# Kernel optimization log

Measured on AMD Instinct MI355X. Metric: run time of the kernel, lower is better.

## Reference

```python
import jax, jax.numpy as jnp
import numpy as np

N = 100000      # nodes
E = 640000      # edges
VOCAB = 100     # Embedding(num_embeddings=100)
EMB = 10        # embed_dim
H = 128         # GCN hidden width


def gcn_conv(x, W, b, src, dst, n):
    """PyG GCNConv: linear (no bias) -> add self loops -> sym-normalized scatter-add -> +bias."""
    x = x @ W                                  # [n, out]
    loop = jnp.arange(n, dtype=src.dtype)
    src2 = jnp.concatenate([src, loop])        # [E+n]
    dst2 = jnp.concatenate([dst, loop])
    deg = jax.ops.segment_sum(jnp.ones_like(dst2, dtype=x.dtype), dst2, num_segments=n)
    dinv = jnp.where(deg > 0, jax.lax.rsqrt(deg), 0.0)
    norm = dinv[src2] * dinv[dst2]             # [E+n]
    out = jax.ops.segment_sum(x[src2] * norm[:, None], dst2, num_segments=n)
    return out + b


def setup_inputs() -> dict:
    key = jax.random.key(0)
    ks = jax.random.split(key, 9)
    x = jax.random.randint(ks[0], (N, 1), 0, VOCAB, dtype=jnp.int32)
    edge_index = jax.random.randint(ks[1], (2, E), 0, N, dtype=jnp.int32)
    batch = jnp.zeros((N,), dtype=jnp.int32)
    emb = jax.random.normal(ks[2], (VOCAB, EMB), dtype=jnp.float32)
    W1 = jax.random.normal(ks[3], (EMB, H), dtype=jnp.float32) * 0.1
    b1 = jnp.zeros((H,), dtype=jnp.float32)
    W2 = jax.random.normal(ks[4], (H, H), dtype=jnp.float32) * 0.1
    b2 = jnp.zeros((H,), dtype=jnp.float32)
    W3 = jax.random.normal(ks[5], (H, 1), dtype=jnp.float32) * 0.1
    b3 = jnp.zeros((1,), dtype=jnp.float32)
    return {"x": x, "edge_index": edge_index, "batch": batch,
            "emb": emb, "W1": W1, "b1": b1, "W2": W2, "b2": b2, "W3": W3, "b3": b3}


def reference(x, edge_index, batch, emb, W1, b1, W2, b2, W3, b3):
    # eval mode: dropout(p=0.5) is identity
    h = emb[x[:, 0]]                           # [N, EMB] embedding lookup + squeeze
    src, dst = edge_index[0], edge_index[1]
    n = h.shape[0]
    h = jax.nn.relu(gcn_conv(h, W1, b1, src, dst, n))   # [N, 128]
    h = jax.nn.relu(gcn_conv(h, W2, b2, src, dst, n))   # [N, 128]
    out = jax.nn.sigmoid((h @ W3 + b3).reshape(-1))      # [N]
    return out
```

## Files before the change

kernel.cpp:

```cpp
#include <hip/hip_runtime.h>
#include <math.h>

#define HDIM 128
#define EMBD 10
#define CAP  64
#define ZSTRIDE 136

typedef __attribute__((ext_vector_type(8))) short short8;
typedef __attribute__((ext_vector_type(8))) unsigned short ushort8;
typedef __attribute__((ext_vector_type(4))) float float4a;
typedef __attribute__((ext_vector_type(4))) unsigned uint4a;

__device__ inline ushort bf16_rne(float f) {
    unsigned u = __float_as_uint(f);
    unsigned r = (u + 0x7fffu + ((u >> 16) & 1u)) >> 16;
    return (ushort)r;
}
__device__ inline float bf16_to_f(ushort u) {
    return __uint_as_float(((unsigned)u) << 16);
}
__device__ inline void acc_row(float* acc, uint4a y, float wt) {
#pragma unroll
    for (int i = 0; i < 4; ++i) {
        unsigned u = y[i];
        acc[2 * i]     += wt * __uint_as_float(u << 16);
        acc[2 * i + 1] += wt * __uint_as_float(u & 0xffff0000u);
    }
}

__global__ void k_prep(const float* __restrict__ emb, const float* __restrict__ W1,
                       const float* __restrict__ W2, ushort* __restrict__ Tb,
                       ushort* __restrict__ W2t, int* __restrict__ cnt,
                       int N, int vocab) {
    int t = blockIdx.x * 256 + threadIdx.x;
    if (t < N) cnt[t] = 0;
    if (t < vocab * HDIM) {
        int c = t >> 7, f = t & 127;
        float s = 0.f;
#pragma unroll
        for (int k = 0; k < EMBD; ++k) s += emb[c * EMBD + k] * W1[k * HDIM + f];
        Tb[t] = bf16_rne(s);
    }
    if (t < HDIM * HDIM) {
        int n = t >> 7, k = t & 127;
        W2t[t] = bf16_rne(W2[k * HDIM + n]);
    }
}

__global__ void k_fill(const int* __restrict__ src, const int* __restrict__ dst,
                       int* __restrict__ cnt, int* __restrict__ slot, int E) {
    int e = blockIdx.x * blockDim.x + threadIdx.x;
    if (e >= E) return;
    int d = dst[e];
    int p = atomicAdd(&cnt[d], 1);
    if (p < CAP) slot[(size_t)d * CAP + p] = src[e];
}

__global__ void k_meta(const int* __restrict__ x, const int* __restrict__ cnt,
                       unsigned* __restrict__ meta, int N) {
    int v = blockIdx.x * 256 + threadIdx.x;
    if (v >= N) return;
    meta[v] = ((unsigned)x[v] << 16) | (unsigned)bf16_rne(rsqrtf((float)cnt[v] + 1.0f));
}

__global__ __launch_bounds__(512) void k_gather1(const int* __restrict__ slot,
                                                 const int* __restrict__ cnt,
                                                 const unsigned* __restrict__ meta,
                                                 const ushort* __restrict__ Tb,
                                                 const float* __restrict__ b1,
                                                 ushort* __restrict__ Ap,
                                                 int N, int vocab) {
    __shared__ ushort TbL[100 * HDIM];
    int n8 = (vocab * HDIM) >> 3;
    for (int i = threadIdx.x; i < n8; i += 512)
        ((ushort8*)TbL)[i] = ((const ushort8*)Tb)[i];
    __syncthreads();

    int tid = blockIdx.x * 512 + threadIdx.x;
    int v = tid >> 4, q = tid & 15;
    if (v >= N) return;
    int deg = cnt[v];
    int m = min(deg, CAP);
    float dv = rsqrtf((float)deg + 1.0f);
    int total = m + 1;
    const int* slotv = slot + (size_t)v * CAP;

    float acc[8] = {0.f, 0.f, 0.f, 0.f, 0.f, 0.f, 0.f, 0.f};
    for (int base = 0; base < total; base += 8) {
        int4 sa = *(const int4*)(slotv + base);
        int4 sb = *(const int4*)(slotv + base + 4);
        int sv[8] = {sa.x, sa.y, sa.z, sa.w, sb.x, sb.y, sb.z, sb.w};
        const unsigned* mp[8];
#pragma unroll
        for (int t = 0; t < 8; ++t) {
            int idx = base + t;
            mp[t] = meta + ((idx < m) ? sv[t] : v);
        }
        unsigned m0, m1, m2, m3, m4, m5, m6, m7;
        asm volatile(
            "global_load_dword %0, %8, off\n\t"
            "global_load_dword %1, %9, off\n\t"
            "global_load_dword %2, %10, off\n\t"
            "global_load_dword %3, %11, off\n\t"
            "global_load_dword %4, %12, off\n\t"
            "global_load_dword %5, %13, off\n\t"
            "global_load_dword %6, %14, off\n\t"
            "global_load_dword %7, %15, off\n\t"
            "s_waitcnt vmcnt(0)"
            : "=&v"(m0), "=&v"(m1), "=&v"(m2), "=&v"(m3),
              "=&v"(m4), "=&v"(m5), "=&v"(m6), "=&v"(m7)
            : "v"(mp[0]), "v"(mp[1]), "v"(mp[2]), "v"(mp[3]),
              "v"(mp[4]), "v"(mp[5]), "v"(mp[6]), "v"(mp[7]));
        unsigned mm[8] = {m0, m1, m2, m3, m4, m5, m6, m7};
#pragma unroll
        for (int t = 0; t < 8; ++t) {
            float wt = (base + t <= m) ? bf16_to_f((ushort)(mm[t] & 0xffffu)) : 0.f;
            ushort8 y = *(const ushort8*)&TbL[(mm[t] >> 16) * HDIM + q * 8];
#pragma unroll
            for (int k = 0; k < 8; ++k) acc[k] += wt * bf16_to_f(y[k]);
        }
    }
    float4 bb0 = *(const float4*)(b1 + q * 8);
    float4 bb1 = *(const float4*)(b1 + q * 8 + 4);
    float bb[8] = {bb0.x, bb0.y, bb0.z, bb0.w, bb1.x, bb1.y, bb1.z, bb1.w};
    ushort8 o;
#pragma unroll
    for (int k = 0; k < 8; ++k)
        o[k] = bf16_rne(dv * fmaxf(dv * acc[k] + bb[k], 0.f));
    *(ushort8*)(Ap + (size_t)v * HDIM + q * 8) = o;
}

__global__ __launch_bounds__(256, 4) void k_conv2(const int* __restrict__ slot,
                                                  const int* __restrict__ cnt,
                                                  const ushort* __restrict__ Ap,
                                                  const ushort* __restrict__ W2t,
                                                  const float* __restrict__ b2,
                                                  const float* __restrict__ W3,
                                                  const float* __restrict__ b3,
                                                  float* __restrict__ out, int N) {
    __shared__ ushort Z[16 * ZSTRIDE];
    __shared__ float pbuf[4][16];
    int tid = threadIdx.x;
    int g = tid >> 4, q = tid & 15;
    int v0 = blockIdx.x * 16;
    int v = min(v0 + g, N - 1);

    int deg = cnt[v];
    int m = min(deg, CAP);
    float dv = rsqrtf((float)deg + 1.0f);
    int total = m + 1;
    const int* slotv = slot + (size_t)v * CAP;
    const ushort* aq = Ap + q * 8;

    float acc[8] = {0.f, 0.f, 0.f, 0.f, 0.f, 0.f, 0.f, 0.f};
    for (int base = 0; base < total; base += 8) {
        int4 sa = *(const int4*)(slotv + base);
        int4 sb = *(const int4*)(slotv + base + 4);
        int sv[8] = {sa.x, sa.y, sa.z, sa.w, sb.x, sb.y, sb.z, sb.w};
        const ushort* pp[8];
#pragma unroll
        for (int t = 0; t < 8; ++t) {
            int idx = base + t;
            int s = (idx < m) ? sv[t] : v;
            pp[t] = aq + (size_t)s * HDIM;
        }
        uint4a r0, r1, r2, r3, r4, r5, r6, r7;
        asm volatile(
            "global_load_dwordx4 %0, %8, off\n\t"
            "global_load_dwordx4 %1, %9, off\n\t"
            "global_load_dwordx4 %2, %10, off\n\t"
            "global_load_dwordx4 %3, %11, off\n\t"
            "global_load_dwordx4 %4, %12, off\n\t"
            "global_load_dwordx4 %5, %13, off\n\t"
            "global_load_dwordx4 %6, %14, off\n\t"
            "global_load_dwordx4 %7, %15, off\n\t"
            "s_waitcnt vmcnt(0)"
            : "=&v"(r0), "=&v"(r1), "=&v"(r2), "=&v"(r3),
              "=&v"(r4), "=&v"(r5), "=&v"(r6), "=&v"(r7)
            : "v"(pp[0]), "v"(pp[1]), "v"(pp[2]), "v"(pp[3]),
              "v"(pp[4]), "v"(pp[5]), "v"(pp[6]), "v"(pp[7]));
        acc_row(acc, r0, (base + 0 <= m) ? 1.f : 0.f);
        acc_row(acc, r1, (base + 1 <= m) ? 1.f : 0.f);
        acc_row(acc, r2, (base + 2 <= m) ? 1.f : 0.f);
        acc_row(acc, r3, (base + 3 <= m) ? 1.f : 0.f);
        acc_row(acc, r4, (base + 4 <= m) ? 1.f : 0.f);
        acc_row(acc, r5, (base + 5 <= m) ? 1.f : 0.f);
        acc_row(acc, r6, (base + 6 <= m) ? 1.f : 0.f);
        acc_row(acc, r7, (base + 7 <= m) ? 1.f : 0.f);
    }
    ushort8 z;
#pragma unroll
    for (int k = 0; k < 8; ++k) z[k] = bf16_rne(dv * acc[k]);
    *(ushort8*)&Z[g * ZSTRIDE + q * 8] = z;
    __syncthreads();

    int lane = tid & 63, w = tid >> 6;
    int l15 = lane & 15, g4 = lane >> 4;
    short8 af[4];
#pragma unroll
    for (int kt = 0; kt < 4; ++kt)
        af[kt] = *(const short8*)&Z[l15 * ZSTRIDE + kt * 32 + g4 * 8];

    float pr[4] = {0.f, 0.f, 0.f, 0.f};
#pragma unroll
    for (int i = 0; i < 2; ++i) {
        int nt = w * 2 + i;
        int col = nt * 16 + l15;
        const ushort* bp = W2t + (size_t)col * HDIM + g4 * 8;
        float4a accD = {0.f, 0.f, 0.f, 0.f};
#pragma unroll
        for (int kt = 0; kt < 4; ++kt) {
            short8 bf = *(const short8*)(bp + kt * 32);
            accD = __builtin_amdgcn_mfma_f32_16x16x32_bf16(af[kt], bf, accD, 0, 0, 0);
        }
        float bc = b2[col], wc = W3[col];
#pragma unroll
        for (int r = 0; r < 4; ++r)
            pr[r] += fmaxf(accD[r] + bc, 0.f) * wc;
    }
#pragma unroll
    for (int off = 1; off < 16; off <<= 1) {
#pragma unroll
        for (int r = 0; r < 4; ++r) pr[r] += __shfl_xor(pr[r], off, 16);
    }
    if (l15 == 0) {
#pragma unroll
        for (int r = 0; r < 4; ++r) pbuf[w][g4 * 4 + r] = pr[r];
    }
    __syncthreads();
    if (tid < 16) {
        int row = tid;
        float s = pbuf[0][row] + pbuf[1][row] + pbuf[2][row] + pbuf[3][row];
        int vr = v0 + row;
        if (vr < N) out[vr] = 1.f / (1.f + expf(-(s + b3[0])));
    }
}

extern "C" void kernel_launch(void* const* d_in, const int* in_sizes, int n_in,
                              void* d_out, int out_size, void* d_ws, size_t ws_size,
                              hipStream_t stream) {
    const int*   x    = (const int*)d_in[0];
    const int*   ei   = (const int*)d_in[1];
    const float* emb  = (const float*)d_in[3];
    const float* W1   = (const float*)d_in[4];
    const float* b1   = (const float*)d_in[5];
    const float* W2   = (const float*)d_in[6];
    const float* b2   = (const float*)d_in[7];
    const float* W3   = (const float*)d_in[8];
    const float* b3   = (const float*)d_in[9];
    float*       out  = (float*)d_out;

    int N = in_sizes[0];
    int E = in_sizes[1] / 2;
    int vocab = in_sizes[3] / EMBD;
    const int* src = ei;
    const int* dst = ei + E;

    char* w = (char*)d_ws;
    ushort*   Tb   = (ushort*)w;    w += (size_t)vocab * HDIM * 2;
    ushort*   Ap   = (ushort*)w;    w += (size_t)N * HDIM * 2;
    ushort*   W2t  = (ushort*)w;    w += (size_t)HDIM * HDIM * 2;
    int*      cnt  = (int*)w;       w += (size_t)N * 4;
    unsigned* meta = (unsigned*)w;  w += (size_t)N * 4;
    int*      slot = (int*)w;       w += (size_t)N * CAP * 4 + 64;

    int prep_elems = N;
    if (vocab * HDIM > prep_elems) prep_elems = vocab * HDIM;
    if (HDIM * HDIM > prep_elems) prep_elems = HDIM * HDIM;
    k_prep<<<(prep_elems + 255) / 256, 256, 0, stream>>>(emb, W1, W2, Tb, W2t, cnt, N, vocab);
    k_fill<<<(E + 255) / 256, 256, 0, stream>>>(src, dst, cnt, slot, E);
    k_meta<<<(N + 255) / 256, 256, 0, stream>>>(x, cnt, meta, N);

    int g1blocks = (int)(((long long)N * 16 + 511) / 512);
    k_gather1<<<g1blocks, 512, 0, stream>>>(slot, cnt, meta, Tb, b1, Ap, N, vocab);

    int cblocks = (N + 15) / 16;
    k_conv2<<<cblocks, 256, 0, stream>>>(slot, cnt, Ap, W2t, b2, W3, b3, out, N);
}
```

Before: 182.0 us.

## Replace fixed-capacity neighbor slots with compact CSR built by prefix scan

Replaces the per-node 64-entry slot buckets with an exact CSR adjacency. It is built by an atomic degree count, a three-kernel prefix scan (which also writes the per-node meta word) and an atomic fill pass that yields per-node end offsets. The gather kernels read neighbor indices from the compact CSR array instead of the sparse padded slot table. This shrinks the adjacency footprint and removes the degree cap, but adds an extra pass over edges and several small launches.

```diff
diff --git a/kernel.cpp b/kernel.cpp
--- a/kernel.cpp
+++ b/kernel.cpp
@@ -3,7 +3,6 @@
 
 #define HDIM 128
 #define EMBD 10
-#define CAP  64
 #define ZSTRIDE 136
 
 typedef __attribute__((ext_vector_type(8))) short short8;
@@ -30,10 +29,10 @@
 
 __global__ void k_prep(const float* __restrict__ emb, const float* __restrict__ W1,
                        const float* __restrict__ W2, ushort* __restrict__ Tb,
-                       ushort* __restrict__ W2t, int* __restrict__ cnt,
+                       ushort* __restrict__ W2t, int* __restrict__ deg,
                        int N, int vocab) {
     int t = blockIdx.x * 256 + threadIdx.x;
-    if (t < N) cnt[t] = 0;
+    if (t < N) deg[t] = 0;
     if (t < vocab * HDIM) {
         int c = t >> 7, f = t & 127;
         float s = 0.f;
@@ -47,24 +46,63 @@
     }
 }
 
+__global__ void k_degcount(const int* __restrict__ dst, int* __restrict__ deg, int E) {
+    int i = blockIdx.x * blockDim.x + threadIdx.x;
+    if (i < E) atomicAdd(&deg[dst[i]], 1);
+}
+
+__global__ void k_psum1(int* __restrict__ a, int* __restrict__ partial,
+                        const int* __restrict__ x, unsigned* __restrict__ meta, int N) {
+    __shared__ int sh[256];
+    int t = threadIdx.x;
+    int i = blockIdx.x * 256 + t;
+    int v = (i < N) ? a[i] : 0;
+    if (i < N)
+        meta[i] = ((unsigned)x[i] << 16) | (unsigned)bf16_rne(rsqrtf((float)v + 1.0f));
+    sh[t] = v;
+    __syncthreads();
+#pragma unroll
+    for (int off = 1; off < 256; off <<= 1) {
+        int add = (t >= off) ? sh[t - off] : 0;
+        __syncthreads();
+        sh[t] += add;
+        __syncthreads();
+    }
+    if (i < N) a[i] = sh[t] - v;
+    if (t == 255) partial[blockIdx.x] = sh[255];
+}
+
+__global__ void k_psum2(int* __restrict__ partial, int nb) {
+    __shared__ int sh[512];
+    int t = threadIdx.x;
+    int v = (t < nb) ? partial[t] : 0;
+    sh[t] = v;
+    __syncthreads();
+#pragma unroll
+    for (int off = 1; off < 512; off <<= 1) {
+        int add = (t >= off) ? sh[t - off] : 0;
+        __syncthreads();
+        sh[t] += add;
+        __syncthreads();
+    }
+    if (t < nb) partial[t] = sh[t] - v;
+}
+
+__global__ void k_psum3(int* __restrict__ a, const int* __restrict__ partial, int N) {
+    int i = blockIdx.x * 256 + threadIdx.x;
+    if (i < N) a[i] += partial[blockIdx.x];
+}
+
 __global__ void k_fill(const int* __restrict__ src, const int* __restrict__ dst,
-                       int* __restrict__ cnt, int* __restrict__ slot, int E) {
+                       int* __restrict__ ends, int* __restrict__ csr, int E) {
     int e = blockIdx.x * blockDim.x + threadIdx.x;
     if (e >= E) return;
-    int d = dst[e];
-    int p = atomicAdd(&cnt[d], 1);
-    if (p < CAP) slot[(size_t)d * CAP + p] = src[e];
-}
-
-__global__ void k_meta(const int* __restrict__ x, const int* __restrict__ cnt,
-                       unsigned* __restrict__ meta, int N) {
-    int v = blockIdx.x * 256 + threadIdx.x;
-    if (v >= N) return;
-    meta[v] = ((unsigned)x[v] << 16) | (unsigned)bf16_rne(rsqrtf((float)cnt[v] + 1.0f));
-}
-
-__global__ __launch_bounds__(512) void k_gather1(const int* __restrict__ slot,
-                                                 const int* __restrict__ cnt,
+    int p = atomicAdd(&ends[dst[e]], 1);
+    csr[p] = src[e];
+}
+
+__global__ __launch_bounds__(512) void k_gather1(const int* __restrict__ csr,
+                                                 const int* __restrict__ ends,
                                                  const unsigned* __restrict__ meta,
                                                  const ushort* __restrict__ Tb,
                                                  const float* __restrict__ b1,
@@ -79,22 +117,20 @@
     int tid = blockIdx.x * 512 + threadIdx.x;
     int v = tid >> 4, q = tid & 15;
     if (v >= N) return;
-    int deg = cnt[v];
-    int m = min(deg, CAP);
+    int e1 = ends[v];
+    int e0 = (v == 0) ? 0 : ends[v - 1];
+    int deg = e1 - e0;
     float dv = rsqrtf((float)deg + 1.0f);
-    int total = m + 1;
-    const int* slotv = slot + (size_t)v * CAP;
+    int total = deg + 1;
 
     float acc[8] = {0.f, 0.f, 0.f, 0.f, 0.f, 0.f, 0.f, 0.f};
     for (int base = 0; base < total; base += 8) {
-        int4 sa = *(const int4*)(slotv + base);
-        int4 sb = *(const int4*)(slotv + base + 4);
-        int sv[8] = {sa.x, sa.y, sa.z, sa.w, sb.x, sb.y, sb.z, sb.w};
         const unsigned* mp[8];
 #pragma unroll
         for (int t = 0; t < 8; ++t) {
             int idx = base + t;
-            mp[t] = meta + ((idx < m) ? sv[t] : v);
+            int s = csr[e0 + idx];
+            mp[t] = meta + ((idx < deg) ? s : v);
         }
         unsigned m0, m1, m2, m3, m4, m5, m6, m7;
         asm volatile(
@@ -114,7 +150,7 @@
         unsigned mm[8] = {m0, m1, m2, m3, m4, m5, m6, m7};
 #pragma unroll
         for (int t = 0; t < 8; ++t) {
-            float wt = (base + t <= m) ? bf16_to_f((ushort)(mm[t] & 0xffffu)) : 0.f;
+            float wt = (base + t <= deg) ? bf16_to_f((ushort)(mm[t] & 0xffffu)) : 0.f;
             ushort8 y = *(const ushort8*)&TbL[(mm[t] >> 16) * HDIM + q * 8];
 #pragma unroll
             for (int k = 0; k < 8; ++k) acc[k] += wt * bf16_to_f(y[k]);
@@ -130,8 +166,8 @@
     *(ushort8*)(Ap + (size_t)v * HDIM + q * 8) = o;
 }
 
-__global__ __launch_bounds__(256, 4) void k_conv2(const int* __restrict__ slot,
-                                                  const int* __restrict__ cnt,
+__global__ __launch_bounds__(256, 4) void k_conv2(const int* __restrict__ csr,
+                                                  const int* __restrict__ ends,
                                                   const ushort* __restrict__ Ap,
                                                   const ushort* __restrict__ W2t,
                                                   const float* __restrict__ b2,
@@ -145,23 +181,21 @@
     int v0 = blockIdx.x * 16;
     int v = min(v0 + g, N - 1);
 
-    int deg = cnt[v];
-    int m = min(deg, CAP);
+    int e1 = ends[v];
+    int e0 = (v == 0) ? 0 : ends[v - 1];
+    int deg = e1 - e0;
     float dv = rsqrtf((float)deg + 1.0f);
-    int total = m + 1;
-    const int* slotv = slot + (size_t)v * CAP;
+    int total = deg + 1;
     const ushort* aq = Ap + q * 8;
 
     float acc[8] = {0.f, 0.f, 0.f, 0.f, 0.f, 0.f, 0.f, 0.f};
     for (int base = 0; base < total; base += 8) {
-        int4 sa = *(const int4*)(slotv + base);
-        int4 sb = *(const int4*)(slotv + base + 4);
-        int sv[8] = {sa.x, sa.y, sa.z, sa.w, sb.x, sb.y, sb.z, sb.w};
         const ushort* pp[8];
 #pragma unroll
         for (int t = 0; t < 8; ++t) {
             int idx = base + t;
-            int s = (idx < m) ? sv[t] : v;
+            int s = csr[e0 + idx];
+            s = (idx < deg) ? s : v;
             pp[t] = aq + (size_t)s * HDIM;
         }
         uint4a r0, r1, r2, r3, r4, r5, r6, r7;
@@ -179,14 +213,14 @@
               "=&v"(r4), "=&v"(r5), "=&v"(r6), "=&v"(r7)
             : "v"(pp[0]), "v"(pp[1]), "v"(pp[2]), "v"(pp[3]),
               "v"(pp[4]), "v"(pp[5]), "v"(pp[6]), "v"(pp[7]));
-        acc_row(acc, r0, (base + 0 <= m) ? 1.f : 0.f);
-        acc_row(acc, r1, (base + 1 <= m) ? 1.f : 0.f);
-        acc_row(acc, r2, (base + 2 <= m) ? 1.f : 0.f);
-        acc_row(acc, r3, (base + 3 <= m) ? 1.f : 0.f);
-        acc_row(acc, r4, (base + 4 <= m) ? 1.f : 0.f);
-        acc_row(acc, r5, (base + 5 <= m) ? 1.f : 0.f);
-        acc_row(acc, r6, (base + 6 <= m) ? 1.f : 0.f);
-        acc_row(acc, r7, (base + 7 <= m) ? 1.f : 0.f);
+        acc_row(acc, r0, (base + 0 <= deg) ? 1.f : 0.f);
+        acc_row(acc, r1, (base + 1 <= deg) ? 1.f : 0.f);
+        acc_row(acc, r2, (base + 2 <= deg) ? 1.f : 0.f);
+        acc_row(acc, r3, (base + 3 <= deg) ? 1.f : 0.f);
+        acc_row(acc, r4, (base + 4 <= deg) ? 1.f : 0.f);
+        acc_row(acc, r5, (base + 5 <= deg) ? 1.f : 0.f);
+        acc_row(acc, r6, (base + 6 <= deg) ? 1.f : 0.f);
+        acc_row(acc, r7, (base + 7 <= deg) ? 1.f : 0.f);
     }
     ushort8 z;
 #pragma unroll
@@ -257,23 +291,29 @@
     const int* dst = ei + E;
 
     char* w = (char*)d_ws;
-    ushort*   Tb   = (ushort*)w;    w += (size_t)vocab * HDIM * 2;
-    ushort*   Ap   = (ushort*)w;    w += (size_t)N * HDIM * 2;
-    ushort*   W2t  = (ushort*)w;    w += (size_t)HDIM * HDIM * 2;
-    int*      cnt  = (int*)w;       w += (size_t)N * 4;
-    unsigned* meta = (unsigned*)w;  w += (size_t)N * 4;
-    int*      slot = (int*)w;       w += (size_t)N * CAP * 4 + 64;
-
+    ushort*   Tb      = (ushort*)w;    w += (size_t)vocab * HDIM * 2;
+    ushort*   Ap      = (ushort*)w;    w += (size_t)N * HDIM * 2;
+    ushort*   W2t     = (ushort*)w;    w += (size_t)HDIM * HDIM * 2;
+    int*      ends    = (int*)w;       w += (size_t)N * 4;
+    unsigned* meta    = (unsigned*)w;  w += (size_t)N * 4;
+    int*      partial = (int*)w;       w += 512 * 4;
+    int*      csr     = (int*)w;       w += ((size_t)E + 16) * 4;
+
+    int nb = (N + 255) / 256;
     int prep_elems = N;
     if (vocab * HDIM > prep_elems) prep_elems = vocab * HDIM;
     if (HDIM * HDIM > prep_elems) prep_elems = HDIM * HDIM;
-    k_prep<<<(prep_elems + 255) / 256, 256, 0, stream>>>(emb, W1, W2, Tb, W2t, cnt, N, vocab);
-    k_fill<<<(E + 255) / 256, 256, 0, stream>>>(src, dst, cnt, slot, E);
-    k_meta<<<(N + 255) / 256, 256, 0, stream>>>(x, cnt, meta, N);
+
+    k_prep<<<(prep_elems + 255) / 256, 256, 0, stream>>>(emb, W1, W2, Tb, W2t, ends, N, vocab);
+    k_degcount<<<(E + 255) / 256, 256, 0, stream>>>(dst, ends, E);
+    k_psum1<<<nb, 256, 0, stream>>>(ends, partial, x, meta, N);
+    k_psum2<<<1, 512, 0, stream>>>(partial, nb);
+    k_psum3<<<nb, 256, 0, stream>>>(ends, partial, N);
+    k_fill<<<(E + 255) / 256, 256, 0, stream>>>(src, dst, ends, csr, E);
 
     int g1blocks = (int)(((long long)N * 16 + 511) / 512);
-    k_gather1<<<g1blocks, 512, 0, stream>>>(slot, cnt, meta, Tb, b1, Ap, N, vocab);
+    k_gather1<<<g1blocks, 512, 0, stream>>>(csr, ends, meta, Tb, b1, Ap, N, vocab);
 
     int cblocks = (N + 15) / 16;
-    k_conv2<<<cblocks, 256, 0, stream>>>(slot, cnt, Ap, W2t, b2, W3, b3, out, N);
-}
+    k_conv2<<<cblocks, 256, 0, stream>>>(csr, ends, Ap, W2t, b2, W3, b3, out, N);
+}
```

New measurement: 214.9 us. 1.18x slower.
